# Optimization experiments

Hardware: AMD Instinct MI355X
Metric: run time of the kernel (lower is better)

## Reference

```python
import jax, jax.numpy as jnp
import numpy as np

B, L, DM = 4, 409, 192            # batch, tokens (1 cls + 16 target + 196 template + 196 search), d_model
DI, DS, DR, K, DEPTH = 384, 16, 12, 4, 24   # d_inner=2*DM, d_state, dt_rank=ceil(DM/16), d_conv, depth
EPS = 1e-5


def setup_inputs() -> dict:
    key = jax.random.key(0)
    ks = list(jax.random.split(key, 16))
    def rn(i, shape, s=0.02):
        return jax.random.normal(ks[i], shape, jnp.float32) * s
    # S4D-real init: A = [1..d_state] per channel, stored as log
    A_log = jnp.log(jnp.tile(jnp.arange(1, DS + 1, dtype=jnp.float32), (DEPTH, DI, 1)))
    return {
        "tokens": jax.random.normal(ks[0], (B, L, DM), jnp.float32),
        "norm_w": jnp.ones((DEPTH, DM), jnp.float32),
        "in_proj_w": rn(1, (DEPTH, 2 * DI, DM)),
        "conv_w": rn(2, (DEPTH, DI, 1, K), 0.2),
        "conv_b": jnp.zeros((DEPTH, DI), jnp.float32),
        "conv_w_b": rn(3, (DEPTH, DI, 1, K), 0.2),
        "conv_b_b": jnp.zeros((DEPTH, DI), jnp.float32),
        "x_proj_w": rn(4, (DEPTH, DR + 2 * DS, DI)),
        "x_proj_w_b": rn(5, (DEPTH, DR + 2 * DS, DI)),
        "dt_proj_w": rn(6, (DEPTH, DI, DR), 0.1),
        "dt_bias": rn(7, (DEPTH, DI), 0.5),
        "dt_proj_w_b": rn(8, (DEPTH, DI, DR), 0.1),
        "dt_bias_b": rn(9, (DEPTH, DI), 0.5),
        "A_log": A_log,
        "A_log_b": A_log,
        "D_param": jnp.ones((DEPTH, DI), jnp.float32),
        "D_param_b": jnp.ones((DEPTH, DI), jnp.float32),
        "out_proj_w": rn(10, (DEPTH, DM, DI)),
        "norm_f_w": jnp.ones((DM,), jnp.float32),
    }


def _rms(x, w):
    return x * jax.lax.rsqrt(jnp.mean(x * x, -1, keepdims=True) + EPS) * w


def _causal_conv(x, w, b):
    # x [B,L,DI]; depthwise causal conv1d, kernel K (pad left K-1)
    y = jax.lax.conv_general_dilated(
        jnp.swapaxes(x, 1, 2), w, (1,), [(K - 1, 0)],
        dimension_numbers=("NCH", "OIH", "NCH"), feature_group_count=DI)
    return jnp.swapaxes(y + b[None, :, None], 1, 2)


def _selective_scan(u, delta, A, Bm, Cm, Dp):
    # u,delta [B,L,DI]; A [DI,DS]; Bm,Cm [B,L,DS]; Dp [DI]
    def step(h, inp):
        u_t, d_t, b_t, c_t = inp  # [B,DI],[B,DI],[B,DS],[B,DS]
        h = h * jnp.exp(d_t[..., None] * A) + (d_t * u_t)[..., None] * b_t[:, None, :]
        return h, jnp.einsum("bdn,bn->bd", h, c_t)
    h0 = jnp.zeros((u.shape[0], A.shape[0], A.shape[1]), u.dtype)
    xs = tuple(jnp.swapaxes(t, 0, 1) for t in (u, delta, Bm, Cm))
    _, ys = jax.lax.scan(step, h0, xs)
    return jnp.swapaxes(ys, 0, 1) + u * Dp


def _scan_dir(xin, cw, cb, xpw, dtw, dtb, a_log, dp):
    xf = jax.nn.silu(_causal_conv(xin, cw, cb))
    x_dbl = jnp.einsum("bld,ed->ble", xf, xpw)
    dt, Bm, Cm = jnp.split(x_dbl, [DR, DR + DS], axis=-1)
    dt = jax.nn.softplus(jnp.einsum("blr,dr->bld", dt, dtw) + dtb)
    return _selective_scan(xf, dt, -jnp.exp(a_log), Bm, Cm, dp)


def _mixer(x, p):
    # bimamba v2: forward scan + backward (flipped) scan with separate params
    xz = jnp.einsum("bld,ed->ble", x, p["in_proj_w"])
    xin, z = jnp.split(xz, 2, axis=-1)
    y_f = _scan_dir(xin, p["conv_w"], p["conv_b"], p["x_proj_w"],
                    p["dt_proj_w"], p["dt_bias"], p["A_log"], p["D_param"])
    y_b = _scan_dir(xin[:, ::-1], p["conv_w_b"], p["conv_b_b"], p["x_proj_w_b"],
                    p["dt_proj_w_b"], p["dt_bias_b"], p["A_log_b"], p["D_param_b"])[:, ::-1]
    y = (y_f + y_b) * jax.nn.silu(z) * 0.5   # z-gating + if_divide_out
    return jnp.einsum("ble,de->bld", y, p["out_proj_w"])


def reference(tokens, norm_w, in_proj_w, conv_w, conv_b, conv_w_b, conv_b_b,
              x_proj_w, x_proj_w_b, dt_proj_w, dt_bias, dt_proj_w_b, dt_bias_b,
              A_log, A_log_b, D_param, D_param_b, out_proj_w, norm_f_w):
    stacked = {"norm_w": norm_w, "in_proj_w": in_proj_w,
               "conv_w": conv_w, "conv_b": conv_b, "conv_w_b": conv_w_b, "conv_b_b": conv_b_b,
               "x_proj_w": x_proj_w, "x_proj_w_b": x_proj_w_b,
               "dt_proj_w": dt_proj_w, "dt_bias": dt_bias,
               "dt_proj_w_b": dt_proj_w_b, "dt_bias_b": dt_bias_b,
               "A_log": A_log, "A_log_b": A_log_b,
               "D_param": D_param, "D_param_b": D_param_b,
               "out_proj_w": out_proj_w}

    def layer(carry, p):
        hidden, residual = carry
        residual = residual + hidden          # add (first layer: residual starts at 0)
        h = _rms(residual, p["norm_w"])       # fused_add_norm prenorm path (RMSNorm)
        h = _mixer(h, p)
        return (h, residual), None

    init = (tokens, jnp.zeros_like(tokens))
    (hidden, residual), _ = jax.lax.scan(layer, init, stacked)
    return _rms(residual + hidden, norm_f_w)
```

## Files before the change

kernel.cpp:

```cpp
#include <hip/hip_runtime.h>
#include <math.h>

#define BB     4
#define LLEN   409
#define DMODEL 192
#define DINNER 384
#define DSTATE 16
#define DRANK  12
#define KCONV  4
#define NLAYER 24
#define NROW   (BB*LLEN)
#define EPSF   1e-5f
#define CH2    16
#define NCH2   26

__device__ __forceinline__ float siluf(float x){ return x/(1.f+__expf(-x)); }
__device__ __forceinline__ float softplusf(float x){ return (x>20.f)? x : log1pf(__expf(x)); }

__global__ void k_init(const float* __restrict__ t, float* __restrict__ r, int n){
  int i = blockIdx.x*256+threadIdx.x;
  if (i<n) r[i]=t[i];
}

__global__ void k_transpose(const float* __restrict__ src, float* __restrict__ dst, int R, int C){
  int total = NLAYER*R*C;
  for (int i = blockIdx.x*blockDim.x+threadIdx.x; i<total; i += gridDim.x*blockDim.x){
    int l = i/(R*C); int rem = i%(R*C); int r = rem/C; int c = rem%C;
    dst[((size_t)l*C + c)*R + r] = src[i];
  }
}

__global__ void k_xpose_pad(const float* __restrict__ src, float* __restrict__ dst){
  int total = NLAYER*DINNER*64;
  for (int i = blockIdx.x*blockDim.x+threadIdx.x; i<total; i += gridDim.x*blockDim.x){
    int l = i/(DINNER*64); int rem = i%(DINNER*64); int c = rem/64; int r = rem%64;
    dst[i] = (r<44)? src[((size_t)l*44 + r)*DINNER + c] : 0.f;
  }
}

__global__ void k_negexpT(const float* __restrict__ a, float* __restrict__ o, int n){
  int i = blockIdx.x*256+threadIdx.x;
  if (i<n){
    int l = i/(DINNER*DSTATE); int rem = i%(DINNER*DSTATE);
    int d = rem/DSTATE, nn = rem%DSTATE;
    o[(size_t)l*DINNER*DSTATE + nn*DINNER + d] = -expf(a[i]);
  }
}

__global__ __launch_bounds__(256) void k_prenorm(const float* __restrict__ residual,
    const float* __restrict__ norm_w, float* __restrict__ xn){
  int wv = threadIdx.x>>6, lane = threadIdx.x&63;
  int row = blockIdx.x*4 + wv;
  if (row >= NROW) return;
  float v[3]; float s = 0.f;
  #pragma unroll
  for (int q=0;q<3;q++){ v[q] = residual[(size_t)row*DMODEL + lane + q*64]; s += v[q]*v[q]; }
  #pragma unroll
  for (int off=1; off<64; off<<=1) s += __shfl_xor(s, off, 64);
  float sc = rsqrtf(s/(float)DMODEL + EPSF);
  #pragma unroll
  for (int q=0;q<3;q++) xn[(size_t)row*DMODEL + lane + q*64] = v[q]*sc*norm_w[lane + q*64];
}

__global__ __launch_bounds__(256) void k_gemm_in(const float* __restrict__ xn,
    const float* __restrict__ Wt, float* __restrict__ xz){
  __shared__ __align__(16) float w_lds[192*64];
  __shared__ __align__(16) float a_lds[192*20];
  int tid = threadIdx.x, r0 = blockIdx.x*16, c0 = blockIdx.y*64;
  {
    int j4 = (tid&15)*4, kr = tid>>4;
    #pragma unroll
    for (int s=0;s<12;s++){
      int k = kr + s*16;
      *reinterpret_cast<float4*>(&w_lds[k*64+j4]) =
        *reinterpret_cast<const float4*>(&Wt[(size_t)k*768 + c0 + j4]);
    }
  }
  {
    int i = tid>>4, kc = (tid&15)*12;
    int row = r0+i;
    #pragma unroll
    for (int m=0;m<12;m+=4){
      float4 v = make_float4(0.f,0.f,0.f,0.f);
      if (row<NROW) v = *reinterpret_cast<const float4*>(&xn[(size_t)row*192 + kc + m]);
      a_lds[(kc+m+0)*20+i]=v.x; a_lds[(kc+m+1)*20+i]=v.y;
      a_lds[(kc+m+2)*20+i]=v.z; a_lds[(kc+m+3)*20+i]=v.w;
    }
  }
  __syncthreads();
  int j = tid & 63, rg = tid >> 6;
  float acc[4] = {0.f,0.f,0.f,0.f};
  #pragma unroll 8
  for (int k=0;k<192;k++){
    float w = w_lds[k*64+j];
    float4 a = *reinterpret_cast<const float4*>(&a_lds[k*20 + rg*4]);
    acc[0]+=a.x*w; acc[1]+=a.y*w; acc[2]+=a.z*w; acc[3]+=a.w*w;
  }
  #pragma unroll
  for (int q=0;q<4;q++){
    int row = r0 + rg*4 + q;
    if (row<NROW) xz[(size_t)row*768 + c0 + j] = acc[q];
  }
}

__global__ __launch_bounds__(256) void k_conv(const float* __restrict__ xz,
    const float* __restrict__ cwf, const float* __restrict__ cbf,
    const float* __restrict__ cwb, const float* __restrict__ cbb,
    float* __restrict__ xf_f, float* __restrict__ xf_b){
  int idx = blockIdx.x*256 + threadIdx.x;
  if (idx >= NROW*(DINNER/4)) return;
  int d4 = (idx % (DINNER/4))*4; int bl = idx / (DINNER/4);
  int b = bl / LLEN; int l = bl % LLEN;
  int dir = blockIdx.y;
  const float* cw = dir? cwb : cwf;
  const float* cb = dir? cbb : cbf;
  float4 w0 = *reinterpret_cast<const float4*>(&cw[(d4+0)*KCONV]);
  float4 w1 = *reinterpret_cast<const float4*>(&cw[(d4+1)*KCONV]);
  float4 w2 = *reinterpret_cast<const float4*>(&cw[(d4+2)*KCONV]);
  float4 w3 = *reinterpret_cast<const float4*>(&cw[(d4+3)*KCONV]);
  float4 acc = *reinterpret_cast<const float4*>(&cb[d4]);
  const float* wa0 = (const float*)&w0; const float* wa1 = (const float*)&w1;
  const float* wa2 = (const float*)&w2; const float* wa3 = (const float*)&w3;
  #pragma unroll
  for (int k=0;k<KCONV;k++){
    int o = dir? (LLEN-1-l-k+3) : (l-3+k);
    bool ok = dir? (l+k>=3) : (o>=0);
    if (ok){
      float4 x = *reinterpret_cast<const float4*>(&xz[((size_t)(b*LLEN+o))*768 + d4]);
      acc.x += wa0[k]*x.x; acc.y += wa1[k]*x.y; acc.z += wa2[k]*x.z; acc.w += wa3[k]*x.w;
    }
  }
  float* out = dir? xf_b : xf_f;
  float4 r; r.x = siluf(acc.x); r.y = siluf(acc.y); r.z = siluf(acc.z); r.w = siluf(acc.w);
  *reinterpret_cast<float4*>(&out[(size_t)bl*DINNER + d4]) = r;
}

__global__ __launch_bounds__(256) void k_xp2(
    const float* __restrict__ xf_f, const float* __restrict__ xf_b,
    const float* __restrict__ WxpPF, const float* __restrict__ WxpPB,
    const float* __restrict__ WdtF, const float* __restrict__ WdtB,
    const float* __restrict__ dtbF, const float* __restrict__ dtbB,
    float* __restrict__ dtbc_f, float* __restrict__ dtbc_b,
    float* __restrict__ dt_f, float* __restrict__ dt_b){
  __shared__ __align__(16) float w_lds[192*64];
  __shared__ __align__(16) float a_lds[192*20];
  __shared__ float dtin_s[16*12];
  int dir = blockIdx.z;
  const float* xf  = dir? xf_b : xf_f;
  const float* Wxp = dir? WxpPB : WxpPF;
  const float* Wdt = dir? WdtB : WdtF;
  const float* dtb = dir? dtbB : dtbF;
  float* dtbc = dir? dtbc_b : dtbc_f;
  float* dtp  = dir? dt_b  : dt_f;
  int tid = threadIdx.x, r0 = blockIdx.x*16;
  int j = tid & 63, rg = tid >> 6;
  float acc[4] = {0.f,0.f,0.f,0.f};
  for (int c=0;c<2;c++){
    int K0 = c*192;
    if (c) __syncthreads();
    {
      int j4 = (tid&15)*4, kr = tid>>4;
      #pragma unroll
      for (int s=0;s<12;s++){
        int k = kr + s*16;
        *reinterpret_cast<float4*>(&w_lds[k*64+j4]) =
          *reinterpret_cast<const float4*>(&Wxp[(size_t)(K0+k)*64 + j4]);
      }
    }
    {
      int i = tid>>4, kc = (tid&15)*12;
      int row = r0+i;
      #pragma unroll
      for (int m=0;m<12;m+=4){
        float4 v = make_float4(0.f,0.f,0.f,0.f);
        if (row<NROW) v = *reinterpret_cast<const float4*>(&xf[(size_t)row*DINNER + K0 + kc + m]);
        a_lds[(kc+m+0)*20+i]=v.x; a_lds[(kc+m+1)*20+i]=v.y;
        a_lds[(kc+m+2)*20+i]=v.z; a_lds[(kc+m+3)*20+i]=v.w;
      }
    }
    __syncthreads();
    #pragma unroll 8
    for (int k=0;k<192;k++){
      float w = w_lds[k*64+j];
      float4 a = *reinterpret_cast<const float4*>(&a_lds[k*20 + rg*4]);
      acc[0]+=a.x*w; acc[1]+=a.y*w; acc[2]+=a.z*w; acc[3]+=a.w*w;
    }
  }
  __syncthreads();
  #pragma unroll
  for (int q=0;q<4;q++){
    int i = rg*4+q, row = r0+i;
    if (j<44 && row<NROW) dtbc[(size_t)row*44 + j] = acc[q];
    if (j<12) dtin_s[i*12 + j] = acc[q];
  }
  __syncthreads();
  for (int idx=tid; idx<12*DINNER; idx+=256) w_lds[idx] = Wdt[idx];
  __syncthreads();
  for (int idx=tid; idx<16*DINNER; idx+=256){
    int i = idx/DINNER, dd = idx - i*DINNER;
    int row = r0+i;
    float v = dtb[dd];
    #pragma unroll
    for (int r=0;r<12;r++) v += dtin_s[i*12+r]*w_lds[r*DINNER+dd];
    if (row<NROW) dtp[(size_t)row*DINNER+dd] = softplusf(v);
  }
}

__global__ __launch_bounds__(128) void k_scan1(
    const float* __restrict__ xf_f, const float* __restrict__ xf_b,
    const float* __restrict__ dtbc_f, const float* __restrict__ dtbc_b,
    const float* __restrict__ dt_f, const float* __restrict__ dt_b,
    const float* __restrict__ anF, const float* __restrict__ anB,
    float* __restrict__ q_buf, float* __restrict__ sdt_buf){
  int dir = blockIdx.z;
  int b  = blockIdx.y / NCH2;
  int ch = blockIdx.y % NCH2;
  const float* xf   = dir? xf_b  : xf_f;
  const float* dtbc = dir? dtbc_b: dtbc_f;
  const float* dtp  = dir? dt_b  : dt_f;
  const float* an   = dir? anB   : anF;
  int t0 = ch*CH2;
  int T  = (t0+CH2<=LLEN)? CH2 : (LLEN-t0);
  int d0 = blockIdx.x*128;
  size_t base = (size_t)b*LLEN + t0;
  __shared__ float dt_s[CH2*128], u_s[CH2*128];
  __shared__ __align__(16) float B_s[CH2*16];
  int tid = threadIdx.x;
  for (int t=0;t<T;t++){
    dt_s[t*128+tid] = dtp[(base+t)*DINNER + d0 + tid];
    u_s [t*128+tid] = xf [(base+t)*DINNER + d0 + tid];
  }
  for (int idx = tid; idx < T*16; idx += 128){
    int t = idx>>4, n = idx&15;
    B_s[idx] = dtbc[(base+t)*44 + 12 + n];
  }
  __syncthreads();
  int d = d0 + tid;
  float A[16], h[16];
  #pragma unroll
  for (int n=0;n<16;n++){ A[n] = an[n*DINNER + d]; h[n] = 0.f; }
  float sdt = 0.f;
  for (int t=0;t<T;t++){
    float dtv = dt_s[t*128+tid];
    float du  = dtv * u_s[t*128+tid];
    float Bv[16];
    #pragma unroll
    for (int q=0;q<4;q++) *reinterpret_cast<float4*>(&Bv[q*4]) =
        *reinterpret_cast<const float4*>(&B_s[t*16 + q*4]);
    #pragma unroll
    for (int n=0;n<16;n++) h[n] = h[n]*__expf(dtv*A[n]) + du*Bv[n];
    sdt += dtv;
  }
  size_t ci = ((size_t)dir*BB + b)*NCH2 + ch;
  float* qo = &q_buf[(ci*DINNER + d)*DSTATE];
  #pragma unroll
  for (int q=0;q<4;q++) *reinterpret_cast<float4*>(&qo[q*4]) =
      make_float4(h[q*4+0], h[q*4+1], h[q*4+2], h[q*4+3]);
  sdt_buf[ci*DINNER + d] = sdt;
}

__global__ __launch_bounds__(256) void k_carry(
    const float* __restrict__ anF, const float* __restrict__ anB,
    float* __restrict__ q_buf, const float* __restrict__ sdt_buf){
  int g = blockIdx.x*256 + threadIdx.x;
  int n = g & 15; int r1 = g >> 4;
  int d = r1 % DINNER; int r2 = r1 / DINNER;
  int b = r2 & 3; int dir = r2 >> 2;
  const float* an = dir? anB : anF;
  float A = an[n*DINNER + d];
  size_t sbase = ((size_t)dir*BB + b)*NCH2;
  float h = 0.f;
  for (int cc=0; cc<NCH2; cc++){
    size_t qi = ((sbase+cc)*DINNER + d)*DSTATE + n;
    float qv = q_buf[qi];
    float sv = sdt_buf[(sbase+cc)*DINNER + d];
    q_buf[qi] = h;
    h = qv + __expf(A*sv)*h;
  }
}

__global__ __launch_bounds__(128) void k_scan2(
    const float* __restrict__ xf_f, const float* __restrict__ xf_b,
    const float* __restrict__ dtbc_f, const float* __restrict__ dtbc_b,
    const float* __restrict__ dt_f, const float* __restrict__ dt_b,
    const float* __restrict__ anF, const float* __restrict__ anB,
    const float* __restrict__ DpF, const float* __restrict__ DpB,
    const float* __restrict__ q_buf,
    float* __restrict__ y_fo, float* __restrict__ y_bo){
  int dir = blockIdx.z;
  int b  = blockIdx.y / NCH2;
  int ch = blockIdx.y % NCH2;
  const float* xf   = dir? xf_b  : xf_f;
  const float* dtbc = dir? dtbc_b: dtbc_f;
  const float* dtp  = dir? dt_b  : dt_f;
  const float* an   = dir? anB   : anF;
  const float* Dp   = dir? DpB   : DpF;
  float* y = dir? y_bo : y_fo;
  int t0 = ch*CH2;
  int T  = (t0+CH2<=LLEN)? CH2 : (LLEN-t0);
  int d0 = blockIdx.x*128;
  size_t base = (size_t)b*LLEN + t0;
  __shared__ float dt_s[CH2*128], u_s[CH2*128];
  __shared__ __align__(16) float B_s[CH2*16], C_s[CH2*16];
  int tid = threadIdx.x;
  for (int t=0;t<T;t++){
    dt_s[t*128+tid] = dtp[(base+t)*DINNER + d0 + tid];
    u_s [t*128+tid] = xf [(base+t)*DINNER + d0 + tid];
  }
  for (int idx = tid; idx < T*16; idx += 128){
    int t = idx>>4, n = idx&15;
    B_s[idx] = dtbc[(base+t)*44 + 12 + n];
    C_s[idx] = dtbc[(base+t)*44 + 28 + n];
  }
  __syncthreads();
  int d = d0 + tid;
  size_t ci = ((size_t)dir*BB + b)*NCH2 + ch;
  const float* qi = &q_buf[(ci*DINNER + d)*DSTATE];
  float A[16], h[16];
  #pragma unroll
  for (int q=0;q<4;q++){
    float4 hv = *reinterpret_cast<const float4*>(&qi[q*4]);
    h[q*4+0]=hv.x; h[q*4+1]=hv.y; h[q*4+2]=hv.z; h[q*4+3]=hv.w;
  }
  #pragma unroll
  for (int n=0;n<16;n++) A[n] = an[n*DINNER + d];
  float Dd = Dp[d];
  for (int t=0;t<T;t++){
    float dtv = dt_s[t*128+tid];
    float u   = u_s [t*128+tid];
    float du  = dtv*u;
    float Bv[16], Cv[16];
    #pragma unroll
    for (int q=0;q<4;q++){
      *reinterpret_cast<float4*>(&Bv[q*4]) = *reinterpret_cast<const float4*>(&B_s[t*16+q*4]);
      *reinterpret_cast<float4*>(&Cv[q*4]) = *reinterpret_cast<const float4*>(&C_s[t*16+q*4]);
    }
    float y0=0.f, y1=0.f, y2=0.f, y3=0.f;
    #pragma unroll
    for (int n=0;n<16;n+=4){
      h[n+0] = h[n+0]*__expf(dtv*A[n+0]) + du*Bv[n+0];
      h[n+1] = h[n+1]*__expf(dtv*A[n+1]) + du*Bv[n+1];
      h[n+2] = h[n+2]*__expf(dtv*A[n+2]) + du*Bv[n+2];
      h[n+3] = h[n+3]*__expf(dtv*A[n+3]) + du*Bv[n+3];
      y0 += h[n+0]*Cv[n+0]; y1 += h[n+1]*Cv[n+1];
      y2 += h[n+2]*Cv[n+2]; y3 += h[n+3]*Cv[n+3];
    }
    y[(base+t)*DINNER + d] = (y0+y1)+(y2+y3) + u*Dd;
  }
}

__global__ __launch_bounds__(256) void k_gate(
    const float* __restrict__ y_f, const float* __restrict__ y_b,
    const float* __restrict__ xz, float* __restrict__ g){
  int idx = blockIdx.x*256 + threadIdx.x;
  if (idx >= NROW*(DINNER/4)) return;
  int d4 = (idx % (DINNER/4))*4; int row = idx / (DINNER/4);
  int b = row/LLEN, l = row%LLEN;
  int rrow = b*LLEN + (LLEN-1-l);
  float4 yf = *reinterpret_cast<const float4*>(&y_f[(size_t)row*DINNER + d4]);
  float4 yb = *reinterpret_cast<const float4*>(&y_b[(size_t)rrow*DINNER + d4]);
  float4 z  = *reinterpret_cast<const float4*>(&xz[(size_t)row*768 + DINNER + d4]);
  float4 r;
  r.x = (yf.x+yb.x)*siluf(z.x)*0.5f; r.y = (yf.y+yb.y)*siluf(z.y)*0.5f;
  r.z = (yf.z+yb.z)*siluf(z.z)*0.5f; r.w = (yf.w+yb.w)*siluf(z.w)*0.5f;
  *reinterpret_cast<float4*>(&g[(size_t)row*DINNER + d4]) = r;
}

__global__ __launch_bounds__(256) void k_gemm_out(const float* __restrict__ g,
    const float* __restrict__ Wt, float* __restrict__ residual){
  __shared__ __align__(16) float w_lds[192*64];
  __shared__ __align__(16) float a_lds[192*20];
  int tid = threadIdx.x, r0 = blockIdx.x*16, c0 = blockIdx.y*64;
  int j = tid & 63, rg = tid >> 6;
  float acc[4] = {0.f,0.f,0.f,0.f};
  for (int c=0;c<2;c++){
    int K0 = c*192;
    if (c) __syncthreads();
    {
      int j4 = (tid&15)*4, kr = tid>>4;
      #pragma unroll
      for (int s=0;s<12;s++){
        int k = kr + s*16;
        *reinterpret_cast<float4*>(&w_lds[k*64+j4]) =
          *reinterpret_cast<const float4*>(&Wt[(size_t)(K0+k)*192 + c0 + j4]);
      }
    }
    {
      int i = tid>>4, kc = (tid&15)*12;
      int row = r0+i;
      #pragma unroll
      for (int m=0;m<12;m+=4){
        float4 v = make_float4(0.f,0.f,0.f,0.f);
        if (row<NROW) v = *reinterpret_cast<const float4*>(&g[(size_t)row*DINNER + K0 + kc + m]);
        a_lds[(kc+m+0)*20+i]=v.x; a_lds[(kc+m+1)*20+i]=v.y;
        a_lds[(kc+m+2)*20+i]=v.z; a_lds[(kc+m+3)*20+i]=v.w;
      }
    }
    __syncthreads();
    #pragma unroll 8
    for (int k=0;k<192;k++){
      float w = w_lds[k*64+j];
      float4 a = *reinterpret_cast<const float4*>(&a_lds[k*20 + rg*4]);
      acc[0]+=a.x*w; acc[1]+=a.y*w; acc[2]+=a.z*w; acc[3]+=a.w*w;
    }
  }
  #pragma unroll
  for (int q=0;q<4;q++){
    int row = r0 + rg*4 + q;
    if (row<NROW) residual[(size_t)row*DMODEL + c0 + j] += acc[q];
  }
}

__global__ __launch_bounds__(256) void k_final(const float* __restrict__ residual,
    const float* __restrict__ nfw, float* __restrict__ out){
  int wv = threadIdx.x>>6, lane = threadIdx.x&63;
  int row = blockIdx.x*4 + wv;
  if (row >= NROW) return;
  float v[3]; float s = 0.f;
  #pragma unroll
  for (int q=0;q<3;q++){ v[q] = residual[(size_t)row*DMODEL + lane + q*64]; s += v[q]*v[q]; }
  #pragma unroll
  for (int off=1; off<64; off<<=1) s += __shfl_xor(s, off, 64);
  float sc = rsqrtf(s/(float)DMODEL + EPSF);
  #pragma unroll
  for (int q=0;q<3;q++) out[(size_t)row*DMODEL + lane + q*64] = v[q]*sc*nfw[lane + q*64];
}

extern "C" void kernel_launch(void* const* d_in, const int* in_sizes, int n_in,
                              void* d_out, int out_size, void* d_ws, size_t ws_size,
                              hipStream_t stream){
  const float* tokens     = (const float*)d_in[0];
  const float* norm_w     = (const float*)d_in[1];
  const float* in_proj_w  = (const float*)d_in[2];
  const float* conv_w     = (const float*)d_in[3];
  const float* conv_b     = (const float*)d_in[4];
  const float* conv_w_b   = (const float*)d_in[5];
  const float* conv_b_b   = (const float*)d_in[6];
  const float* x_proj_w   = (const float*)d_in[7];
  const float* x_proj_w_b = (const float*)d_in[8];
  const float* dt_proj_w  = (const float*)d_in[9];
  const float* dt_bias    = (const float*)d_in[10];
  const float* dt_proj_w_b= (const float*)d_in[11];
  const float* dt_bias_b  = (const float*)d_in[12];
  const float* A_log      = (const float*)d_in[13];
  const float* A_log_b    = (const float*)d_in[14];
  const float* D_param    = (const float*)d_in[15];
  const float* D_param_b  = (const float*)d_in[16];
  const float* out_proj_w = (const float*)d_in[17];
  const float* norm_f_w   = (const float*)d_in[18];

  float* ws = (float*)d_ws;
  size_t off = 0;
  float* residual = ws + off; off += (size_t)NROW*DMODEL;
  float* xn       = ws + off; off += (size_t)NROW*DMODEL;
  float* xz       = ws + off; off += (size_t)NROW*768;
  float* xf_f     = ws + off; off += (size_t)NROW*DINNER;
  float* xf_b     = ws + off; off += (size_t)NROW*DINNER;
  float* dtbc_f   = ws + off; off += (size_t)NROW*44;
  float* dtbc_b   = ws + off; off += (size_t)NROW*44;
  float* dt_f     = ws + off; off += (size_t)NROW*DINNER;
  float* dt_b     = ws + off; off += (size_t)NROW*DINNER;
  float* y_f      = ws + off; off += (size_t)NROW*DINNER;
  float* y_b      = ws + off; off += (size_t)NROW*DINNER;
  float* gbuf     = ws + off; off += (size_t)NROW*DINNER;
  float* q_buf    = ws + off; off += (size_t)2*BB*NCH2*DINNER*DSTATE;
  float* sdt_buf  = ws + off; off += (size_t)2*BB*NCH2*DINNER;
  float* WtIn     = ws + off; off += (size_t)NLAYER*DMODEL*768;
  float* WtXpPF   = ws + off; off += (size_t)NLAYER*DINNER*64;
  float* WtXpPB   = ws + off; off += (size_t)NLAYER*DINNER*64;
  float* WtDtF    = ws + off; off += (size_t)NLAYER*DRANK*DINNER;
  float* WtDtB    = ws + off; off += (size_t)NLAYER*DRANK*DINNER;
  float* WtOut    = ws + off; off += (size_t)NLAYER*DINNER*DMODEL;
  float* AnTF     = ws + off; off += (size_t)NLAYER*DINNER*DSTATE;
  float* AnTB     = ws + off; off += (size_t)NLAYER*DINNER*DSTATE;
  if (off*sizeof(float) > ws_size) return;

  k_init<<<dim3((NROW*DMODEL+255)/256),256,0,stream>>>(tokens, residual, NROW*DMODEL);
  k_transpose<<<2048,256,0,stream>>>(in_proj_w,  WtIn,  768, DMODEL);
  k_xpose_pad<<<1024,256,0,stream>>>(x_proj_w,   WtXpPF);
  k_xpose_pad<<<1024,256,0,stream>>>(x_proj_w_b, WtXpPB);
  k_transpose<<<512, 256,0,stream>>>(dt_proj_w,  WtDtF, DINNER, DRANK);
  k_transpose<<<512, 256,0,stream>>>(dt_proj_w_b,WtDtB, DINNER, DRANK);
  k_transpose<<<2048,256,0,stream>>>(out_proj_w, WtOut, DMODEL, DINNER);
  k_negexpT<<<dim3((NLAYER*DINNER*DSTATE+255)/256),256,0,stream>>>(A_log,   AnTF, NLAYER*DINNER*DSTATE);
  k_negexpT<<<dim3((NLAYER*DINNER*DSTATE+255)/256),256,0,stream>>>(A_log_b, AnTB, NLAYER*DINNER*DSTATE);

  const int RT16 = (NROW+15)/16;
  const int EW4  = (NROW*(DINNER/4)+255)/256;
  for (int l=0; l<NLAYER; l++){
    k_prenorm<<<dim3((NROW+3)/4),256,0,stream>>>(residual, norm_w + (size_t)l*DMODEL, xn);
    k_gemm_in<<<dim3(RT16,12),256,0,stream>>>(xn, WtIn + (size_t)l*DMODEL*768, xz);
    k_conv<<<dim3(EW4,2),256,0,stream>>>(xz,
        conv_w + (size_t)l*DINNER*KCONV, conv_b + (size_t)l*DINNER,
        conv_w_b + (size_t)l*DINNER*KCONV, conv_b_b + (size_t)l*DINNER, xf_f, xf_b);
    k_xp2<<<dim3(RT16,1,2),256,0,stream>>>(xf_f, xf_b,
        WtXpPF + (size_t)l*DINNER*64, WtXpPB + (size_t)l*DINNER*64,
        WtDtF + (size_t)l*DRANK*DINNER, WtDtB + (size_t)l*DRANK*DINNER,
        dt_bias + (size_t)l*DINNER, dt_bias_b + (size_t)l*DINNER,
        dtbc_f, dtbc_b, dt_f, dt_b);
    k_scan1<<<dim3(3,BB*NCH2,2),128,0,stream>>>(xf_f, xf_b, dtbc_f, dtbc_b, dt_f, dt_b,
        AnTF + (size_t)l*DINNER*DSTATE, AnTB + (size_t)l*DINNER*DSTATE, q_buf, sdt_buf);
    k_carry<<<dim3(192),256,0,stream>>>(
        AnTF + (size_t)l*DINNER*DSTATE, AnTB + (size_t)l*DINNER*DSTATE, q_buf, sdt_buf);
    k_scan2<<<dim3(3,BB*NCH2,2),128,0,stream>>>(xf_f, xf_b, dtbc_f, dtbc_b, dt_f, dt_b,
        AnTF + (size_t)l*DINNER*DSTATE, AnTB + (size_t)l*DINNER*DSTATE,
        D_param + (size_t)l*DINNER, D_param_b + (size_t)l*DINNER,
        q_buf, y_f, y_b);
    k_gate<<<dim3(EW4),256,0,stream>>>(y_f, y_b, xz, gbuf);
    k_gemm_out<<<dim3(RT16,3),256,0,stream>>>(gbuf, WtOut + (size_t)l*DINNER*DMODEL, residual);
  }
  k_final<<<dim3((NROW+3)/4),256,0,stream>>>(residual, norm_f_w, (float*)d_out);
}
```

Measured before the change: 2.458 ms.

## Fuse prenorm into in-proj GEMM, conv into x-proj, gate into out-proj; tile transposes

Merges RMSNorm into the input-projection GEMM prologue, computes the causal conv plus SiLU inside the x-projection kernel's tile load, and folds the gating into the out-projection's A-tile load. This drops three launches and the xn and gbuf intermediates per layer. The one-time weight transposes now use an LDS-tiled kernel, and the A_log negexp is rewritten with coalesced writes. The cost is redundant work: the norm is recomputed by each of the 12 column blocks, the gate by each of the 3 output blocks, and the conv loads are scalar rather than float4.

```diff
diff --git a/kernel.cpp b/kernel.cpp
--- a/kernel.cpp
+++ b/kernel.cpp
@@ -22,51 +22,48 @@
   if (i<n) r[i]=t[i];
 }
 
-__global__ void k_transpose(const float* __restrict__ src, float* __restrict__ dst, int R, int C){
-  int total = NLAYER*R*C;
-  for (int i = blockIdx.x*blockDim.x+threadIdx.x; i<total; i += gridDim.x*blockDim.x){
-    int l = i/(R*C); int rem = i%(R*C); int r = rem/C; int c = rem%C;
-    dst[((size_t)l*C + c)*R + r] = src[i];
-  }
-}
-
-__global__ void k_xpose_pad(const float* __restrict__ src, float* __restrict__ dst){
-  int total = NLAYER*DINNER*64;
-  for (int i = blockIdx.x*blockDim.x+threadIdx.x; i<total; i += gridDim.x*blockDim.x){
-    int l = i/(DINNER*64); int rem = i%(DINNER*64); int c = rem/64; int r = rem%64;
-    dst[i] = (r<44)? src[((size_t)l*44 + r)*DINNER + c] : 0.f;
-  }
-}
-
-__global__ void k_negexpT(const float* __restrict__ a, float* __restrict__ o, int n){
+__global__ __launch_bounds__(256) void k_txp(const float* __restrict__ src,
+    float* __restrict__ dst, int R, int C, int RP){
+  __shared__ float t[32][33];
+  int l = blockIdx.z;
+  int c0 = blockIdx.x*32, r0 = blockIdx.y*32;
+  const float* s = src + (size_t)l*R*C;
+  float* d = dst + (size_t)l*C*RP;
+  int tx = threadIdx.x, ty = threadIdx.y;
+  #pragma unroll
+  for (int yy=ty; yy<32; yy+=8){
+    int rr = r0+yy, cc = c0+tx;
+    t[yy][tx] = (rr<R && cc<C)? s[(size_t)rr*C+cc] : 0.f;
+  }
+  __syncthreads();
+  #pragma unroll
+  for (int yy=ty; yy<32; yy+=8){
+    int cc = c0+yy, rr = r0+tx;
+    if (cc<C && rr<RP) d[(size_t)cc*RP+rr] = t[tx][yy];
+  }
+}
+
+__global__ void k_negexpT2(const float* __restrict__ a, float* __restrict__ o, int n){
   int i = blockIdx.x*256+threadIdx.x;
   if (i<n){
     int l = i/(DINNER*DSTATE); int rem = i%(DINNER*DSTATE);
-    int d = rem/DSTATE, nn = rem%DSTATE;
-    o[(size_t)l*DINNER*DSTATE + nn*DINNER + d] = -expf(a[i]);
-  }
-}
-
-__global__ __launch_bounds__(256) void k_prenorm(const float* __restrict__ residual,
-    const float* __restrict__ norm_w, float* __restrict__ xn){
-  int wv = threadIdx.x>>6, lane = threadIdx.x&63;
-  int row = blockIdx.x*4 + wv;
-  if (row >= NROW) return;
-  float v[3]; float s = 0.f;
-  #pragma unroll
-  for (int q=0;q<3;q++){ v[q] = residual[(size_t)row*DMODEL + lane + q*64]; s += v[q]*v[q]; }
-  #pragma unroll
-  for (int off=1; off<64; off<<=1) s += __shfl_xor(s, off, 64);
-  float sc = rsqrtf(s/(float)DMODEL + EPSF);
-  #pragma unroll
-  for (int q=0;q<3;q++) xn[(size_t)row*DMODEL + lane + q*64] = v[q]*sc*norm_w[lane + q*64];
-}
-
-__global__ __launch_bounds__(256) void k_gemm_in(const float* __restrict__ xn,
-    const float* __restrict__ Wt, float* __restrict__ xz){
+    int nn = rem/DINNER, d = rem%DINNER;
+    o[i] = -expf(a[((size_t)l*DINNER + d)*DSTATE + nn]);
+  }
+}
+
+__global__ __launch_bounds__(256) void k_normin(const float* __restrict__ residual,
+    const float* __restrict__ norm_w, const float* __restrict__ Wt,
+    float* __restrict__ xz){
   __shared__ __align__(16) float w_lds[192*64];
   __shared__ __align__(16) float a_lds[192*20];
+  __shared__ float rs_s[16];
   int tid = threadIdx.x, r0 = blockIdx.x*16, c0 = blockIdx.y*64;
+  #pragma unroll
+  for (int s=0;s<12;s++){
+    int idx = tid + s*256; int i = idx/DMODEL, k = idx%DMODEL; int row = r0+i;
+    a_lds[k*20+i] = (row<NROW)? residual[(size_t)row*DMODEL+k] : 0.f;
+  }
   {
     int j4 = (tid&15)*4, kr = tid>>4;
     #pragma unroll
@@ -76,16 +73,29 @@
         *reinterpret_cast<const float4*>(&Wt[(size_t)k*768 + c0 + j4]);
     }
   }
+  __syncthreads();
+  int wv = tid>>6, lane = tid&63;
   {
-    int i = tid>>4, kc = (tid&15)*12;
-    int row = r0+i;
-    #pragma unroll
-    for (int m=0;m<12;m+=4){
-      float4 v = make_float4(0.f,0.f,0.f,0.f);
-      if (row<NROW) v = *reinterpret_cast<const float4*>(&xn[(size_t)row*192 + kc + m]);
-      a_lds[(kc+m+0)*20+i]=v.x; a_lds[(kc+m+1)*20+i]=v.y;
-      a_lds[(kc+m+2)*20+i]=v.z; a_lds[(kc+m+3)*20+i]=v.w;
-    }
+    float ss[4] = {0.f,0.f,0.f,0.f};
+    #pragma unroll
+    for (int q=0;q<3;q++){
+      int k = lane + q*64;
+      #pragma unroll
+      for (int r=0;r<4;r++){ float v = a_lds[k*20 + wv*4 + r]; ss[r] += v*v; }
+    }
+    #pragma unroll
+    for (int r=0;r<4;r++){
+      float s = ss[r];
+      #pragma unroll
+      for (int off=1; off<64; off<<=1) s += __shfl_xor(s, off, 64);
+      if (lane==0) rs_s[wv*4+r] = rsqrtf(s/(float)DMODEL + EPSF);
+    }
+  }
+  __syncthreads();
+  #pragma unroll
+  for (int s=0;s<12;s++){
+    int idx = tid + s*256; int k = idx>>4, i = idx&15;
+    a_lds[k*20+i] *= rs_s[i]*norm_w[k];
   }
   __syncthreads();
   int j = tid & 63, rg = tid >> 6;
@@ -103,54 +113,28 @@
   }
 }
 
-__global__ __launch_bounds__(256) void k_conv(const float* __restrict__ xz,
+__global__ __launch_bounds__(256) void k_convxp(
+    const float* __restrict__ xz,
     const float* __restrict__ cwf, const float* __restrict__ cbf,
     const float* __restrict__ cwb, const float* __restrict__ cbb,
-    float* __restrict__ xf_f, float* __restrict__ xf_b){
-  int idx = blockIdx.x*256 + threadIdx.x;
-  if (idx >= NROW*(DINNER/4)) return;
-  int d4 = (idx % (DINNER/4))*4; int bl = idx / (DINNER/4);
-  int b = bl / LLEN; int l = bl % LLEN;
-  int dir = blockIdx.y;
-  const float* cw = dir? cwb : cwf;
-  const float* cb = dir? cbb : cbf;
-  float4 w0 = *reinterpret_cast<const float4*>(&cw[(d4+0)*KCONV]);
-  float4 w1 = *reinterpret_cast<const float4*>(&cw[(d4+1)*KCONV]);
-  float4 w2 = *reinterpret_cast<const float4*>(&cw[(d4+2)*KCONV]);
-  float4 w3 = *reinterpret_cast<const float4*>(&cw[(d4+3)*KCONV]);
-  float4 acc = *reinterpret_cast<const float4*>(&cb[d4]);
-  const float* wa0 = (const float*)&w0; const float* wa1 = (const float*)&w1;
-  const float* wa2 = (const float*)&w2; const float* wa3 = (const float*)&w3;
-  #pragma unroll
-  for (int k=0;k<KCONV;k++){
-    int o = dir? (LLEN-1-l-k+3) : (l-3+k);
-    bool ok = dir? (l+k>=3) : (o>=0);
-    if (ok){
-      float4 x = *reinterpret_cast<const float4*>(&xz[((size_t)(b*LLEN+o))*768 + d4]);
-      acc.x += wa0[k]*x.x; acc.y += wa1[k]*x.y; acc.z += wa2[k]*x.z; acc.w += wa3[k]*x.w;
-    }
-  }
-  float* out = dir? xf_b : xf_f;
-  float4 r; r.x = siluf(acc.x); r.y = siluf(acc.y); r.z = siluf(acc.z); r.w = siluf(acc.w);
-  *reinterpret_cast<float4*>(&out[(size_t)bl*DINNER + d4]) = r;
-}
-
-__global__ __launch_bounds__(256) void k_xp2(
-    const float* __restrict__ xf_f, const float* __restrict__ xf_b,
     const float* __restrict__ WxpPF, const float* __restrict__ WxpPB,
     const float* __restrict__ WdtF, const float* __restrict__ WdtB,
     const float* __restrict__ dtbF, const float* __restrict__ dtbB,
+    float* __restrict__ xf_f, float* __restrict__ xf_b,
     float* __restrict__ dtbc_f, float* __restrict__ dtbc_b,
     float* __restrict__ dt_f, float* __restrict__ dt_b){
   __shared__ __align__(16) float w_lds[192*64];
   __shared__ __align__(16) float a_lds[192*20];
+  __shared__ float cw_s[192*4], cb_s[192];
   __shared__ float dtin_s[16*12];
   int dir = blockIdx.z;
-  const float* xf  = dir? xf_b : xf_f;
-  const float* Wxp = dir? WxpPB : WxpPF;
+  const float* cw  = dir? cwb  : cwf;
+  const float* cb  = dir? cbb  : cbf;
+  const float* Wxp = dir? WxpPB: WxpPF;
   const float* Wdt = dir? WdtB : WdtF;
   const float* dtb = dir? dtbB : dtbF;
-  float* dtbc = dir? dtbc_b : dtbc_f;
+  float* xf   = dir? xf_b  : xf_f;
+  float* dtbc = dir? dtbc_b: dtbc_f;
   float* dtp  = dir? dt_b  : dt_f;
   int tid = threadIdx.x, r0 = blockIdx.x*16;
   int j = tid & 63, rg = tid >> 6;
@@ -158,6 +142,8 @@
   for (int c=0;c<2;c++){
     int K0 = c*192;
     if (c) __syncthreads();
+    for (int idx=tid; idx<192*4; idx+=256) cw_s[idx] = cw[K0*4 + idx];
+    if (tid<192) cb_s[tid] = cb[K0 + tid];
     {
       int j4 = (tid&15)*4, kr = tid>>4;
       #pragma unroll
@@ -167,16 +153,26 @@
           *reinterpret_cast<const float4*>(&Wxp[(size_t)(K0+k)*64 + j4]);
       }
     }
-    {
-      int i = tid>>4, kc = (tid&15)*12;
+    __syncthreads();
+    #pragma unroll
+    for (int s=0;s<12;s++){
+      int idx = tid + s*256; int i = idx/192, k = idx - i*192;
       int row = r0+i;
-      #pragma unroll
-      for (int m=0;m<12;m+=4){
-        float4 v = make_float4(0.f,0.f,0.f,0.f);
-        if (row<NROW) v = *reinterpret_cast<const float4*>(&xf[(size_t)row*DINNER + K0 + kc + m]);
-        a_lds[(kc+m+0)*20+i]=v.x; a_lds[(kc+m+1)*20+i]=v.y;
-        a_lds[(kc+m+2)*20+i]=v.z; a_lds[(kc+m+3)*20+i]=v.w;
+      float v = 0.f;
+      if (row<NROW){
+        int b = row/LLEN, l = row - b*LLEN;
+        float a0 = cb_s[k];
+        #pragma unroll
+        for (int kk=0;kk<4;kk++){
+          int o; bool ok;
+          if (dir==0){ o = l-3+kk; ok = (o>=0); }
+          else       { o = LLEN-1-l-kk+3; ok = (l+kk>=3); }
+          if (ok) a0 += cw_s[k*4+kk]*xz[((size_t)(b*LLEN+o))*768 + K0 + k];
+        }
+        v = siluf(a0);
+        xf[(size_t)row*DINNER + K0 + k] = v;
       }
+      a_lds[k*20+i] = v;
     }
     __syncthreads();
     #pragma unroll 8
@@ -349,25 +345,10 @@
   }
 }
 
-__global__ __launch_bounds__(256) void k_gate(
+__global__ __launch_bounds__(256) void k_gateout(
     const float* __restrict__ y_f, const float* __restrict__ y_b,
-    const float* __restrict__ xz, float* __restrict__ g){
-  int idx = blockIdx.x*256 + threadIdx.x;
-  if (idx >= NROW*(DINNER/4)) return;
-  int d4 = (idx % (DINNER/4))*4; int row = idx / (DINNER/4);
-  int b = row/LLEN, l = row%LLEN;
-  int rrow = b*LLEN + (LLEN-1-l);
-  float4 yf = *reinterpret_cast<const float4*>(&y_f[(size_t)row*DINNER + d4]);
-  float4 yb = *reinterpret_cast<const float4*>(&y_b[(size_t)rrow*DINNER + d4]);
-  float4 z  = *reinterpret_cast<const float4*>(&xz[(size_t)row*768 + DINNER + d4]);
-  float4 r;
-  r.x = (yf.x+yb.x)*siluf(z.x)*0.5f; r.y = (yf.y+yb.y)*siluf(z.y)*0.5f;
-  r.z = (yf.z+yb.z)*siluf(z.z)*0.5f; r.w = (yf.w+yb.w)*siluf(z.w)*0.5f;
-  *reinterpret_cast<float4*>(&g[(size_t)row*DINNER + d4]) = r;
-}
-
-__global__ __launch_bounds__(256) void k_gemm_out(const float* __restrict__ g,
-    const float* __restrict__ Wt, float* __restrict__ residual){
+    const float* __restrict__ xz, const float* __restrict__ Wt,
+    float* __restrict__ residual){
   __shared__ __align__(16) float w_lds[192*64];
   __shared__ __align__(16) float a_lds[192*20];
   int tid = threadIdx.x, r0 = blockIdx.x*16, c0 = blockIdx.y*64;
@@ -385,16 +366,19 @@
           *reinterpret_cast<const float4*>(&Wt[(size_t)(K0+k)*192 + c0 + j4]);
       }
     }
-    {
-      int i = tid>>4, kc = (tid&15)*12;
-      int row = r0+i;
-      #pragma unroll
-      for (int m=0;m<12;m+=4){
-        float4 v = make_float4(0.f,0.f,0.f,0.f);
-        if (row<NROW) v = *reinterpret_cast<const float4*>(&g[(size_t)row*DINNER + K0 + kc + m]);
-        a_lds[(kc+m+0)*20+i]=v.x; a_lds[(kc+m+1)*20+i]=v.y;
-        a_lds[(kc+m+2)*20+i]=v.z; a_lds[(kc+m+3)*20+i]=v.w;
+    #pragma unroll
+    for (int s=0;s<12;s++){
+      int idx = tid + s*256; int i = idx/192, k = idx - i*192;
+      int row = r0+i; float v = 0.f;
+      if (row<NROW){
+        int b = row/LLEN, l = row - b*LLEN;
+        int rrow = b*LLEN + (LLEN-1-l);
+        float yf = y_f[(size_t)row*DINNER + K0 + k];
+        float yb = y_b[(size_t)rrow*DINNER + K0 + k];
+        float z  = xz[(size_t)row*768 + DINNER + K0 + k];
+        v = (yf+yb)*siluf(z)*0.5f;
       }
+      a_lds[k*20+i] = v;
     }
     __syncthreads();
     #pragma unroll 8
@@ -452,7 +436,6 @@
   float* ws = (float*)d_ws;
   size_t off = 0;
   float* residual = ws + off; off += (size_t)NROW*DMODEL;
-  float* xn       = ws + off; off += (size_t)NROW*DMODEL;
   float* xz       = ws + off; off += (size_t)NROW*768;
   float* xf_f     = ws + off; off += (size_t)NROW*DINNER;
   float* xf_b     = ws + off; off += (size_t)NROW*DINNER;
@@ -462,7 +445,6 @@
   float* dt_b     = ws + off; off += (size_t)NROW*DINNER;
   float* y_f      = ws + off; off += (size_t)NROW*DINNER;
   float* y_b      = ws + off; off += (size_t)NROW*DINNER;
-  float* gbuf     = ws + off; off += (size_t)NROW*DINNER;
   float* q_buf    = ws + off; off += (size_t)2*BB*NCH2*DINNER*DSTATE;
   float* sdt_buf  = ws + off; off += (size_t)2*BB*NCH2*DINNER;
   float* WtIn     = ws + off; off += (size_t)NLAYER*DMODEL*768;
@@ -476,28 +458,27 @@
   if (off*sizeof(float) > ws_size) return;
 
   k_init<<<dim3((NROW*DMODEL+255)/256),256,0,stream>>>(tokens, residual, NROW*DMODEL);
-  k_transpose<<<2048,256,0,stream>>>(in_proj_w,  WtIn,  768, DMODEL);
-  k_xpose_pad<<<1024,256,0,stream>>>(x_proj_w,   WtXpPF);
-  k_xpose_pad<<<1024,256,0,stream>>>(x_proj_w_b, WtXpPB);
-  k_transpose<<<512, 256,0,stream>>>(dt_proj_w,  WtDtF, DINNER, DRANK);
-  k_transpose<<<512, 256,0,stream>>>(dt_proj_w_b,WtDtB, DINNER, DRANK);
-  k_transpose<<<2048,256,0,stream>>>(out_proj_w, WtOut, DMODEL, DINNER);
-  k_negexpT<<<dim3((NLAYER*DINNER*DSTATE+255)/256),256,0,stream>>>(A_log,   AnTF, NLAYER*DINNER*DSTATE);
-  k_negexpT<<<dim3((NLAYER*DINNER*DSTATE+255)/256),256,0,stream>>>(A_log_b, AnTB, NLAYER*DINNER*DSTATE);
+  dim3 tb(32,8);
+  k_txp<<<dim3(6,24,NLAYER),tb,0,stream>>>(in_proj_w,  WtIn,   768, 192, 768);
+  k_txp<<<dim3(12,2,NLAYER),tb,0,stream>>>(x_proj_w,   WtXpPF,  44, 384,  64);
+  k_txp<<<dim3(12,2,NLAYER),tb,0,stream>>>(x_proj_w_b, WtXpPB,  44, 384,  64);
+  k_txp<<<dim3(1,12,NLAYER),tb,0,stream>>>(dt_proj_w,  WtDtF,  384,  12, 384);
+  k_txp<<<dim3(1,12,NLAYER),tb,0,stream>>>(dt_proj_w_b,WtDtB,  384,  12, 384);
+  k_txp<<<dim3(12,6,NLAYER),tb,0,stream>>>(out_proj_w, WtOut,  192, 384, 192);
+  k_negexpT2<<<dim3((NLAYER*DINNER*DSTATE+255)/256),256,0,stream>>>(A_log,   AnTF, NLAYER*DINNER*DSTATE);
+  k_negexpT2<<<dim3((NLAYER*DINNER*DSTATE+255)/256),256,0,stream>>>(A_log_b, AnTB, NLAYER*DINNER*DSTATE);
 
   const int RT16 = (NROW+15)/16;
-  const int EW4  = (NROW*(DINNER/4)+255)/256;
   for (int l=0; l<NLAYER; l++){
-    k_prenorm<<<dim3((NROW+3)/4),256,0,stream>>>(residual, norm_w + (size_t)l*DMODEL, xn);
-    k_gemm_in<<<dim3(RT16,12),256,0,stream>>>(xn, WtIn + (size_t)l*DMODEL*768, xz);
-    k_conv<<<dim3(EW4,2),256,0,stream>>>(xz,
+    k_normin<<<dim3(RT16,12),256,0,stream>>>(residual, norm_w + (size_t)l*DMODEL,
+        WtIn + (size_t)l*DMODEL*768, xz);
+    k_convxp<<<dim3(RT16,1,2),256,0,stream>>>(xz,
         conv_w + (size_t)l*DINNER*KCONV, conv_b + (size_t)l*DINNER,
-        conv_w_b + (size_t)l*DINNER*KCONV, conv_b_b + (size_t)l*DINNER, xf_f, xf_b);
-    k_xp2<<<dim3(RT16,1,2),256,0,stream>>>(xf_f, xf_b,
+        conv_w_b + (size_t)l*DINNER*KCONV, conv_b_b + (size_t)l*DINNER,
         WtXpPF + (size_t)l*DINNER*64, WtXpPB + (size_t)l*DINNER*64,
         WtDtF + (size_t)l*DRANK*DINNER, WtDtB + (size_t)l*DRANK*DINNER,
         dt_bias + (size_t)l*DINNER, dt_bias_b + (size_t)l*DINNER,
-        dtbc_f, dtbc_b, dt_f, dt_b);
+        xf_f, xf_b, dtbc_f, dtbc_b, dt_f, dt_b);
     k_scan1<<<dim3(3,BB*NCH2,2),128,0,stream>>>(xf_f, xf_b, dtbc_f, dtbc_b, dt_f, dt_b,
         AnTF + (size_t)l*DINNER*DSTATE, AnTB + (size_t)l*DINNER*DSTATE, q_buf, sdt_buf);
     k_carry<<<dim3(192),256,0,stream>>>(
@@ -506,8 +487,7 @@
         AnTF + (size_t)l*DINNER*DSTATE, AnTB + (size_t)l*DINNER*DSTATE,
         D_param + (size_t)l*DINNER, D_param_b + (size_t)l*DINNER,
         q_buf, y_f, y_b);
-    k_gate<<<dim3(EW4),256,0,stream>>>(y_f, y_b, xz, gbuf);
-    k_gemm_out<<<dim3(RT16,3),256,0,stream>>>(gbuf, WtOut + (size_t)l*DINNER*DMODEL, residual);
+    k_gateout<<<dim3(RT16,3),256,0,stream>>>(y_f, y_b, xz, WtOut + (size_t)l*DINNER*DMODEL, residual);
   }
   k_final<<<dim3((NROW+3)/4),256,0,stream>>>(residual, norm_f_w, (float*)d_out);
 }
```

Result: slower. 3.438 ms (+39.9%).

## Fold chunk carry propagation into scan2 and tile weight transposes

Applied to the files above, without the earlier changes.

Removes the separate k_carry kernel. Each scan2 block now recomputes its incoming state by serially combining all earlier chunk summaries from q_buf and sdt_buf, which saves one launch per layer but adds redundant O(chunks) work in later chunks. The setup weight transposes are replaced by a shared-memory tiled transpose kernel with coalesced reads and writes. The A negexp transpose is rewritten to make its writes coalesced instead of its reads.

```diff
diff --git a/kernel.cpp b/kernel.cpp
--- a/kernel.cpp
+++ b/kernel.cpp
@@ -22,28 +22,33 @@
   if (i<n) r[i]=t[i];
 }
 
-__global__ void k_transpose(const float* __restrict__ src, float* __restrict__ dst, int R, int C){
-  int total = NLAYER*R*C;
-  for (int i = blockIdx.x*blockDim.x+threadIdx.x; i<total; i += gridDim.x*blockDim.x){
-    int l = i/(R*C); int rem = i%(R*C); int r = rem/C; int c = rem%C;
-    dst[((size_t)l*C + c)*R + r] = src[i];
-  }
-}
-
-__global__ void k_xpose_pad(const float* __restrict__ src, float* __restrict__ dst){
-  int total = NLAYER*DINNER*64;
-  for (int i = blockIdx.x*blockDim.x+threadIdx.x; i<total; i += gridDim.x*blockDim.x){
-    int l = i/(DINNER*64); int rem = i%(DINNER*64); int c = rem/64; int r = rem%64;
-    dst[i] = (r<44)? src[((size_t)l*44 + r)*DINNER + c] : 0.f;
-  }
-}
-
-__global__ void k_negexpT(const float* __restrict__ a, float* __restrict__ o, int n){
+__global__ __launch_bounds__(256) void k_txp(const float* __restrict__ src,
+    float* __restrict__ dst, int R, int C, int RP){
+  __shared__ float t[32][33];
+  int l = blockIdx.z;
+  int c0 = blockIdx.x*32, r0 = blockIdx.y*32;
+  const float* s = src + (size_t)l*R*C;
+  float* d = dst + (size_t)l*C*RP;
+  int tx = threadIdx.x, ty = threadIdx.y;
+  #pragma unroll
+  for (int yy=ty; yy<32; yy+=8){
+    int rr = r0+yy, cc = c0+tx;
+    t[yy][tx] = (rr<R && cc<C)? s[(size_t)rr*C+cc] : 0.f;
+  }
+  __syncthreads();
+  #pragma unroll
+  for (int yy=ty; yy<32; yy+=8){
+    int cc = c0+yy, rr = r0+tx;
+    if (cc<C && rr<RP) d[(size_t)cc*RP+rr] = t[tx][yy];
+  }
+}
+
+__global__ void k_negexpT2(const float* __restrict__ a, float* __restrict__ o, int n){
   int i = blockIdx.x*256+threadIdx.x;
   if (i<n){
     int l = i/(DINNER*DSTATE); int rem = i%(DINNER*DSTATE);
-    int d = rem/DSTATE, nn = rem%DSTATE;
-    o[(size_t)l*DINNER*DSTATE + nn*DINNER + d] = -expf(a[i]);
+    int nn = rem/DINNER, d = rem%DINNER;
+    o[i] = -expf(a[((size_t)l*DINNER + d)*DSTATE + nn]);
   }
 }
 
@@ -259,33 +264,13 @@
   sdt_buf[ci*DINNER + d] = sdt;
 }
 
-__global__ __launch_bounds__(256) void k_carry(
-    const float* __restrict__ anF, const float* __restrict__ anB,
-    float* __restrict__ q_buf, const float* __restrict__ sdt_buf){
-  int g = blockIdx.x*256 + threadIdx.x;
-  int n = g & 15; int r1 = g >> 4;
-  int d = r1 % DINNER; int r2 = r1 / DINNER;
-  int b = r2 & 3; int dir = r2 >> 2;
-  const float* an = dir? anB : anF;
-  float A = an[n*DINNER + d];
-  size_t sbase = ((size_t)dir*BB + b)*NCH2;
-  float h = 0.f;
-  for (int cc=0; cc<NCH2; cc++){
-    size_t qi = ((sbase+cc)*DINNER + d)*DSTATE + n;
-    float qv = q_buf[qi];
-    float sv = sdt_buf[(sbase+cc)*DINNER + d];
-    q_buf[qi] = h;
-    h = qv + __expf(A*sv)*h;
-  }
-}
-
 __global__ __launch_bounds__(128) void k_scan2(
     const float* __restrict__ xf_f, const float* __restrict__ xf_b,
     const float* __restrict__ dtbc_f, const float* __restrict__ dtbc_b,
     const float* __restrict__ dt_f, const float* __restrict__ dt_b,
     const float* __restrict__ anF, const float* __restrict__ anB,
     const float* __restrict__ DpF, const float* __restrict__ DpB,
-    const float* __restrict__ q_buf,
+    const float* __restrict__ q_buf, const float* __restrict__ sdt_buf,
     float* __restrict__ y_fo, float* __restrict__ y_bo){
   int dir = blockIdx.z;
   int b  = blockIdx.y / NCH2;
@@ -314,16 +299,20 @@
   }
   __syncthreads();
   int d = d0 + tid;
-  size_t ci = ((size_t)dir*BB + b)*NCH2 + ch;
-  const float* qi = &q_buf[(ci*DINNER + d)*DSTATE];
   float A[16], h[16];
   #pragma unroll
-  for (int q=0;q<4;q++){
-    float4 hv = *reinterpret_cast<const float4*>(&qi[q*4]);
-    h[q*4+0]=hv.x; h[q*4+1]=hv.y; h[q*4+2]=hv.z; h[q*4+3]=hv.w;
-  }
-  #pragma unroll
-  for (int n=0;n<16;n++) A[n] = an[n*DINNER + d];
+  for (int n=0;n<16;n++){ A[n] = an[n*DINNER + d]; h[n] = 0.f; }
+  size_t sbase = ((size_t)dir*BB + b)*NCH2;
+  for (int cc=0; cc<ch; cc++){
+    float sv = sdt_buf[(sbase+cc)*DINNER + d];
+    const float* qp = &q_buf[((sbase+cc)*DINNER + d)*DSTATE];
+    float qv[16];
+    #pragma unroll
+    for (int q=0;q<4;q++) *reinterpret_cast<float4*>(&qv[q*4]) =
+        *reinterpret_cast<const float4*>(&qp[q*4]);
+    #pragma unroll
+    for (int n=0;n<16;n++) h[n] = qv[n] + __expf(A[n]*sv)*h[n];
+  }
   float Dd = Dp[d];
   for (int t=0;t<T;t++){
     float dtv = dt_s[t*128+tid];
@@ -476,14 +465,15 @@
   if (off*sizeof(float) > ws_size) return;
 
   k_init<<<dim3((NROW*DMODEL+255)/256),256,0,stream>>>(tokens, residual, NROW*DMODEL);
-  k_transpose<<<2048,256,0,stream>>>(in_proj_w,  WtIn,  768, DMODEL);
-  k_xpose_pad<<<1024,256,0,stream>>>(x_proj_w,   WtXpPF);
-  k_xpose_pad<<<1024,256,0,stream>>>(x_proj_w_b, WtXpPB);
-  k_transpose<<<512, 256,0,stream>>>(dt_proj_w,  WtDtF, DINNER, DRANK);
-  k_transpose<<<512, 256,0,stream>>>(dt_proj_w_b,WtDtB, DINNER, DRANK);
-  k_transpose<<<2048,256,0,stream>>>(out_proj_w, WtOut, DMODEL, DINNER);
-  k_negexpT<<<dim3((NLAYER*DINNER*DSTATE+255)/256),256,0,stream>>>(A_log,   AnTF, NLAYER*DINNER*DSTATE);
-  k_negexpT<<<dim3((NLAYER*DINNER*DSTATE+255)/256),256,0,stream>>>(A_log_b, AnTB, NLAYER*DINNER*DSTATE);
+  dim3 tb(32,8);
+  k_txp<<<dim3(6,24,NLAYER),tb,0,stream>>>(in_proj_w,  WtIn,   768, 192, 768);
+  k_txp<<<dim3(12,2,NLAYER),tb,0,stream>>>(x_proj_w,   WtXpPF,  44, 384,  64);
+  k_txp<<<dim3(12,2,NLAYER),tb,0,stream>>>(x_proj_w_b, WtXpPB,  44, 384,  64);
+  k_txp<<<dim3(1,12,NLAYER),tb,0,stream>>>(dt_proj_w,  WtDtF,  384,  12, 384);
+  k_txp<<<dim3(1,12,NLAYER),tb,0,stream>>>(dt_proj_w_b,WtDtB,  384,  12, 384);
+  k_txp<<<dim3(12,6,NLAYER),tb,0,stream>>>(out_proj_w, WtOut,  192, 384, 192);
+  k_negexpT2<<<dim3((NLAYER*DINNER*DSTATE+255)/256),256,0,stream>>>(A_log,   AnTF, NLAYER*DINNER*DSTATE);
+  k_negexpT2<<<dim3((NLAYER*DINNER*DSTATE+255)/256),256,0,stream>>>(A_log_b, AnTB, NLAYER*DINNER*DSTATE);
 
   const int RT16 = (NROW+15)/16;
   const int EW4  = (NROW*(DINNER/4)+255)/256;
@@ -500,12 +490,10 @@
         dtbc_f, dtbc_b, dt_f, dt_b);
     k_scan1<<<dim3(3,BB*NCH2,2),128,0,stream>>>(xf_f, xf_b, dtbc_f, dtbc_b, dt_f, dt_b,
         AnTF + (size_t)l*DINNER*DSTATE, AnTB + (size_t)l*DINNER*DSTATE, q_buf, sdt_buf);
-    k_carry<<<dim3(192),256,0,stream>>>(
-        AnTF + (size_t)l*DINNER*DSTATE, AnTB + (size_t)l*DINNER*DSTATE, q_buf, sdt_buf);
     k_scan2<<<dim3(3,BB*NCH2,2),128,0,stream>>>(xf_f, xf_b, dtbc_f, dtbc_b, dt_f, dt_b,
         AnTF + (size_t)l*DINNER*DSTATE, AnTB + (size_t)l*DINNER*DSTATE,
         D_param + (size_t)l*DINNER, D_param_b + (size_t)l*DINNER,
-        q_buf, y_f, y_b);
+        q_buf, sdt_buf, y_f, y_b);
     k_gate<<<dim3(EW4),256,0,stream>>>(y_f, y_b, xz, gbuf);
     k_gemm_out<<<dim3(RT16,3),256,0,stream>>>(gbuf, WtOut + (size_t)l*DINNER*DMODEL, residual);
   }
```

Result: faster. 2.402 ms (-2.3%).
